# Optimization experiments

Measured on AMD Instinct MI355X. Metric: run time of the kernel, lower is better.

Reference implementation:

```python
import math
import jax, jax.numpy as jnp
import numpy as np

V, BS, L, C, H, B, T = 50257, 2048, 4, 768, 12, 2, 2048
D = C // H


def layer_norm(x, g, b, eps=1e-5):
    m = x.mean(-1, keepdims=True)
    v = ((x - m) ** 2).mean(-1, keepdims=True)
    return (x - m) / jnp.sqrt(v + eps) * g + b


def setup_inputs() -> dict:
    key = jax.random.key(0)
    ks = jax.random.split(key, 10)
    s = 0.02
    inp = {}
    inp["idx"] = jax.random.randint(ks[0], (B, T), 0, V)
    inp["tok_emb"] = jax.random.normal(ks[1], (V, C), jnp.float32) * s
    inp["pos_emb"] = jax.random.normal(ks[2], (BS, C), jnp.float32) * s
    inp["ln1_g"] = jnp.ones((L, C)); inp["ln1_b"] = jnp.zeros((L, C))
    inp["qkv_w"] = jax.random.normal(ks[3], (L, C, 3 * C), jnp.float32) * s
    inp["qkv_b"] = jnp.zeros((L, 3 * C))
    inp["aproj_w"] = jax.random.normal(ks[4], (L, C, C), jnp.float32) * s
    inp["aproj_b"] = jnp.zeros((L, C))
    inp["ln2_g"] = jnp.ones((L, C)); inp["ln2_b"] = jnp.zeros((L, C))
    inp["fc_w"] = jax.random.normal(ks[5], (L, C, 4 * C), jnp.float32) * s
    inp["fc_b"] = jnp.zeros((L, 4 * C))
    inp["mproj_w"] = jax.random.normal(ks[6], (L, 4 * C, C), jnp.float32) * s
    inp["mproj_b"] = jnp.zeros((L, C))
    inp["lnf_g"] = jnp.ones((C,)); inp["lnf_b"] = jnp.zeros((C,))
    inp["head_w"] = jax.random.normal(ks[7], (C, V), jnp.float32) * s
    return inp


def reference(idx, tok_emb, pos_emb, ln1_g, ln1_b, qkv_w, qkv_b, aproj_w, aproj_b,
              ln2_g, ln2_b, fc_w, fc_b, mproj_w, mproj_b, lnf_g, lnf_b, head_w):
    b, t = idx.shape
    x = tok_emb[idx] + pos_emb[:t][None]  # [B,T,C]; dropout p=0 -> identity
    mask = jnp.tril(jnp.ones((t, t), bool))  # causal
    neg_inf = jnp.finfo(x.dtype).min
    n_layer = qkv_w.shape[0]
    for l in range(n_layer):
        h = layer_norm(x, ln1_g[l], ln1_b[l])
        qkv = h @ qkv_w[l] + qkv_b[l]  # [B,T,3C]
        q, k, v = jnp.split(qkv, 3, axis=-1)
        q = q.reshape(b, t, H, D).transpose(0, 2, 1, 3)  # [B,H,T,D]
        k = k.reshape(b, t, H, D).transpose(0, 2, 1, 3)
        v = v.reshape(b, t, H, D).transpose(0, 2, 1, 3)
        att = jnp.einsum('bhqd,bhkd->bhqk', q, k) / math.sqrt(D)
        att = jnp.where(mask, att, neg_inf)
        att = jax.nn.softmax(att, axis=-1)
        y = jnp.einsum('bhqk,bhkd->bhqd', att, v)
        y = y.transpose(0, 2, 1, 3).reshape(b, t, C)
        x = x + (y @ aproj_w[l] + aproj_b[l])
        h2 = layer_norm(x, ln2_g[l], ln2_b[l])
        hid = jax.nn.gelu(h2 @ fc_w[l] + fc_b[l], approximate=False)  # exact erf GELU (torch default)
        x = x + (hid @ mproj_w[l] + mproj_b[l])
    x = layer_norm(x, lnf_g, lnf_b)
    logits = x @ head_w  # [B,T,V]
    return logits
```

## Files before the change

kernel.cpp:

```cpp
#include <hip/hip_runtime.h>
#include <cstdint>
#include <cstddef>

#define Tn 2048
#define Bn 2
#define Hn 12
#define Cn 768
#define Ln 4
#define Vn 50257

typedef unsigned short ushort_t;
typedef __attribute__((ext_vector_type(8))) __bf16 bf16x8;
typedef __attribute__((ext_vector_type(8))) unsigned short u16x8;
typedef __attribute__((ext_vector_type(4))) unsigned short u16x4;
typedef __attribute__((ext_vector_type(4))) float f32x4;

static constexpr size_t QKV_ELEMS = (size_t)Bn * Hn * Tn * 64;
static constexpr size_t OFF_QKV = 0;
static constexpr size_t OFF_APROJ = 1769472;
static constexpr size_t OFF_FC = 2359296;
static constexpr size_t OFF_MPROJ = 4718592;

__device__ inline unsigned short f2bf(float f) {
  unsigned int u = __float_as_uint(f);
  unsigned int r = (u + 0x7fffu + ((u >> 16) & 1u)) >> 16;
  return (unsigned short)r;
}

__device__ inline f32x4 zero4() { f32x4 z; z[0]=0.f; z[1]=0.f; z[2]=0.f; z[3]=0.f; return z; }

__device__ inline void gload_lds16(const ushort_t* g, ushort_t* l) {
  __builtin_amdgcn_global_load_lds(
      (const __attribute__((address_space(1))) void*)g,
      (__attribute__((address_space(3))) void*)l, 16, 0, 0);
}

__device__ inline int swz_lin() {
  int nbm = gridDim.x;
  int lin = blockIdx.y * nbm + blockIdx.x;
  int nwg = nbm * gridDim.y;
  int q = nwg >> 3, r = nwg & 7, x = lin & 7, p = lin >> 3;
  return (x < r ? x * (q + 1) : r * (q + 1) + (x - r) * q) + p;
}

__global__ __launch_bounds__(192) void embed_kernel(const int* __restrict__ idx,
    const float* __restrict__ tok, const float* __restrict__ pos, float* __restrict__ x) {
  int row = blockIdx.x;
  int t = row & (Tn - 1);
  int token = idx[row];
  const f32x4* tr = (const f32x4*)(tok + (size_t)token * Cn);
  const f32x4* pr = (const f32x4*)(pos + (size_t)t * Cn);
  f32x4* xr = (f32x4*)(x + (size_t)row * Cn);
  xr[threadIdx.x] = tr[threadIdx.x] + pr[threadIdx.x];
}

__global__ __launch_bounds__(256) void ln_kernel(const float* __restrict__ x,
    const float* __restrict__ gam, const float* __restrict__ bet, ushort_t* __restrict__ out) {
  const int wv = threadIdx.x >> 6, lane = threadIdx.x & 63;
  const int row = blockIdx.x * 4 + wv;
  const f32x4* xr = (const f32x4*)(x + (size_t)row * Cn);
  f32x4 v[3]; float s = 0.f, s2 = 0.f;
  #pragma unroll
  for (int e = 0; e < 3; ++e) {
    v[e] = xr[lane + e*64];
    #pragma unroll
    for (int j = 0; j < 4; ++j) { s += v[e][j]; s2 += v[e][j]*v[e][j]; }
  }
  #pragma unroll
  for (int off = 32; off >= 1; off >>= 1) { s += __shfl_xor(s, off); s2 += __shfl_xor(s2, off); }
  float mean = s * (1.f / Cn);
  float var  = s2 * (1.f / Cn) - mean * mean;
  float rstd = rsqrtf(var + 1e-5f);
  const f32x4* g4 = (const f32x4*)gam;
  const f32x4* b4 = (const f32x4*)bet;
  u16x4* o4 = (u16x4*)(out + (size_t)row * Cn);
  #pragma unroll
  for (int e = 0; e < 3; ++e) {
    f32x4 gv = g4[lane + e*64], bv = b4[lane + e*64];
    u16x4 o;
    #pragma unroll
    for (int j = 0; j < 4; ++j) o[j] = f2bf((v[e][j] - mean) * rstd * gv[j] + bv[j]);
    o4[lane + e*64] = o;
  }
}

__global__ __launch_bounds__(256) void tcvt_kernel(const float* __restrict__ in,
    ushort_t* __restrict__ out, int K, int N, int Npad) {
  __shared__ float tile[32][33];
  int n0 = blockIdx.x * 32, k0 = blockIdx.y * 32;
  int tx = threadIdx.x, ty = threadIdx.y;
  #pragma unroll
  for (int r = 0; r < 4; ++r) {
    int k = k0 + ty + 8*r;
    int n = n0 + tx;
    tile[ty + 8*r][tx] = (n < N) ? in[(size_t)k * N + n] : 0.f;
  }
  __syncthreads();
  #pragma unroll
  for (int r = 0; r < 4; ++r) {
    int n = n0 + ty + 8*r;
    out[(size_t)n * K + k0 + tx] = f2bf(tile[tx][ty + 8*r]);
  }
}

__global__ __launch_bounds__(256) void tcvt4_kernel(const float* __restrict__ qkvp,
    const float* __restrict__ aprojp, const float* __restrict__ fcp,
    const float* __restrict__ mprojp, ushort_t* __restrict__ wT) {
  __shared__ float tile[32][33];
  int bid = blockIdx.x;
  const float* in; int K, N, tilesX, local; size_t ooff;
  if (bid < 1728)      { in = qkvp;   K = 768;  N = 2304; tilesX = 72; ooff = OFF_QKV;   local = bid; }
  else if (bid < 2304) { in = aprojp; K = 768;  N = 768;  tilesX = 24; ooff = OFF_APROJ; local = bid - 1728; }
  else if (bid < 4608) { in = fcp;    K = 768;  N = 3072; tilesX = 96; ooff = OFF_FC;    local = bid - 2304; }
  else                 { in = mprojp; K = 3072; N = 768;  tilesX = 24; ooff = OFF_MPROJ; local = bid - 4608; }
  int n0 = (local % tilesX) * 32, k0 = (local / tilesX) * 32;
  int tx = threadIdx.x, ty = threadIdx.y;
  ushort_t* out = wT + ooff;
  #pragma unroll
  for (int r = 0; r < 4; ++r)
    tile[ty + 8*r][tx] = in[(size_t)(k0 + ty + 8*r) * N + n0 + tx];
  __syncthreads();
  #pragma unroll
  for (int r = 0; r < 4; ++r)
    out[(size_t)(n0 + ty + 8*r) * K + k0 + tx] = f2bf(tile[tx][ty + 8*r]);
}

__global__ __launch_bounds__(256) void vtrans_kernel(const ushort_t* __restrict__ vin,
                                                     ushort_t* __restrict__ vout) {
  __shared__ ushort_t tile[64][65];
  int t0 = blockIdx.x * 64;
  size_t bh = blockIdx.y;
  const ushort_t* src = vin + (bh * Tn + t0) * 64;
  int row = threadIdx.x >> 2, c0 = (threadIdx.x & 3) * 16;
  u16x8 a = *(const u16x8*)&src[(size_t)row * 64 + c0];
  u16x8 b = *(const u16x8*)&src[(size_t)row * 64 + c0 + 8];
  #pragma unroll
  for (int j = 0; j < 8; ++j) { tile[row][c0 + j] = a[j]; tile[row][c0 + 8 + j] = b[j]; }
  __syncthreads();
  int d = threadIdx.x >> 2, tq = (threadIdx.x & 3) * 16;
  u16x8 o0, o1;
  #pragma unroll
  for (int j = 0; j < 8; ++j) { o0[j] = tile[tq + j][d]; o1[j] = tile[tq + 8 + j][d]; }
  ushort_t* dst = vout + (bh * 64 + d) * Tn + t0 + tq;
  *(u16x8*)&dst[0] = o0;
  *(u16x8*)&dst[8] = o1;
}

__global__ __launch_bounds__(512, 2) void gemm256_kernel(
    const ushort_t* __restrict__ A, const ushort_t* __restrict__ Bt,
    const float* __restrict__ bias, float* __restrict__ outp,
    int M, int N, int K) {
  __shared__ ushort_t lds[3 * 16384];
  const int t = threadIdx.x;
  const int w = t >> 6, l = t & 63, lo = l & 15, g = l >> 4;
  const int wm = w >> 2, wn = w & 3;

  int bm, bn;
  {
    int seq = swz_lin();
    int gsz = 8 * gridDim.y;
    int grp = seq / gsz;
    int t2 = seq - grp * gsz;
    bn = t2 >> 3;
    bm = grp * 8 + (t2 & 7);
  }

  const ushort_t* gAb = A  + (size_t)bm * 256 * K;
  const ushort_t* gBb = Bt + (size_t)bn * 256 * K;

  f32x4 acc[8][4];
  #pragma unroll
  for (int i = 0; i < 8; ++i)
    #pragma unroll
    for (int j = 0; j < 4; ++j) acc[i][j] = zero4();

  auto stage = [&](int kt, int buf) {
    const int k0 = kt << 5;
    #pragma unroll
    for (int j = 0; j < 2; ++j) {
      const int q = j * 512 + t;
      const int r = q >> 2;
      const int cc = ((q & 3) ^ ((r >> 1) & 3)) << 3;
      gload_lds16(gAb + (size_t)r * K + k0 + cc,
                  &lds[buf * 16384 + j * 4096 + w * 512]);
      gload_lds16(gBb + (size_t)r * K + k0 + cc,
                  &lds[buf * 16384 + 8192 + j * 4096 + w * 512]);
    }
  };
  const int csw = ((lo >> 1) & 3) << 3;
  auto compute = [&](int buf) {
    const ushort_t* as = &lds[buf * 16384];
    const ushort_t* bs = &lds[buf * 16384 + 8192];
    bf16x8 af[8], bfr[4];
    #pragma unroll
    for (int mi = 0; mi < 8; ++mi)
      af[mi] = *(const bf16x8*)&as[(wm*128 + mi*16 + lo) * 32 + ((g*8) ^ csw)];
    #pragma unroll
    for (int ni = 0; ni < 4; ++ni)
      bfr[ni] = *(const bf16x8*)&bs[(wn*64 + ni*16 + lo) * 32 + ((g*8) ^ csw)];
    __builtin_amdgcn_s_setprio(1);
    #pragma unroll
    for (int mi = 0; mi < 8; ++mi)
      #pragma unroll
      for (int ni = 0; ni < 4; ++ni)
        acc[mi][ni] = __builtin_amdgcn_mfma_f32_16x16x32_bf16(af[mi], bfr[ni], acc[mi][ni], 0, 0, 0);
    __builtin_amdgcn_s_setprio(0);
  };

  const int NK = K >> 5;
  stage(0, 0); stage(1, 1); stage(2, 2);
  asm volatile("s_waitcnt vmcnt(8)" ::: "memory");
  __builtin_amdgcn_s_barrier();

  int buf = 0;
  #pragma unroll 1
  for (int kt = 0; kt < NK; ++kt) {
    compute(buf);
    asm volatile("s_waitcnt lgkmcnt(0)" ::: "memory");
    __builtin_amdgcn_s_barrier();
    if (kt + 3 < NK) {
      stage(kt + 3, buf);
      asm volatile("s_waitcnt vmcnt(8)" ::: "memory");
    } else if (kt + 2 < NK) {
      asm volatile("s_waitcnt vmcnt(4)" ::: "memory");
    } else {
      asm volatile("s_waitcnt vmcnt(0)" ::: "memory");
    }
    __builtin_amdgcn_s_barrier();
    buf = (buf == 2) ? 0 : buf + 1;
  }

  #pragma unroll
  for (int mi = 0; mi < 8; ++mi) {
    #pragma unroll
    for (int ni = 0; ni < 4; ++ni) {
      int colg = bn*256 + wn*64 + ni*16 + lo;
      if (colg < N) {
        float bv = bias ? bias[colg] : 0.f;
        #pragma unroll
        for (int i = 0; i < 4; ++i) {
          int rowg = bm*256 + wm*128 + mi*16 + 4*g + i;
          outp[(size_t)rowg * N + colg] = acc[mi][ni][i] + bv;
        }
      }
    }
  }
}

template<int MODE, int TM>
__global__ __launch_bounds__(256) void gemm_kernel(
    const ushort_t* __restrict__ A, const ushort_t* __restrict__ Bt,
    const float* __restrict__ bias, void* __restrict__ outp,
    const float* __restrict__ res, int M, int N, int K) {
  constexpr int MI = TM / 32;
  constexpr int ASZ = TM * 32;
  constexpr int BUFE = ASZ + 4096;
  constexpr int LPT = TM/64 + 2;
  __shared__ ushort_t lds[3 * BUFE];
  const int t = threadIdx.x;
  int bm, bn;
  {
    int seq = swz_lin();
    const int G = 8;
    int gsz = G * gridDim.y;
    int grp = seq / gsz;
    int t2 = seq - grp * gsz;
    bn = t2 / G;
    bm = grp * G + (t2 - bn * G);
  }
  const int w = t >> 6, l = t & 63, lo = l & 15, g = l >> 4;
  const int wm = w >> 1, wn = w & 1;

  f32x4 acc[MI][4];
  #pragma unroll
  for (int i = 0; i < MI; ++i)
    #pragma unroll
    for (int j = 0; j < 4; ++j) acc[i][j] = zero4();

  const ushort_t* gAb = A  + (size_t)bm * TM * K;
  const ushort_t* gBb = Bt + (size_t)bn * 128 * K;

  auto stage = [&](int kt, int buf) {
    const int k0 = kt << 5;
    #pragma unroll
    for (int j = 0; j < TM/64; ++j) {
      const int q = j * 256 + t;
      const int r = q >> 2;
      const int cc = ((q & 3) ^ ((r >> 1) & 3)) << 3;
      gload_lds16(gAb + (size_t)r * K + k0 + cc, &lds[buf*BUFE + (j*256 + w*64)*8]);
    }
    #pragma unroll
    for (int j = 0; j < 2; ++j) {
      const int q = j * 256 + t;
      const int r = q >> 2;
      const int cc = ((q & 3) ^ ((r >> 1) & 3)) << 3;
      gload_lds16(gBb + (size_t)r * K + k0 + cc, &lds[buf*BUFE + ASZ + (j*256 + w*64)*8]);
    }
  };
  const int csw = ((lo >> 1) & 3) << 3;
  auto compute = [&](int buf) {
    const ushort_t* as = &lds[buf * BUFE];
    const ushort_t* bs = &lds[buf * BUFE + ASZ];
    bf16x8 af[MI], bfr[4];
    #pragma unroll
    for (int mi = 0; mi < MI; ++mi)
      af[mi] = *(const bf16x8*)&as[(wm*(TM/2) + mi*16 + lo) * 32 + ((g*8) ^ csw)];
    #pragma unroll
    for (int ni = 0; ni < 4; ++ni)
      bfr[ni] = *(const bf16x8*)&bs[(wn*64 + ni*16 + lo) * 32 + ((g*8) ^ csw)];
    __builtin_amdgcn_s_setprio(1);
    #pragma unroll
    for (int mi = 0; mi < MI; ++mi)
      #pragma unroll
      for (int ni = 0; ni < 4; ++ni)
        acc[mi][ni] = __builtin_amdgcn_mfma_f32_16x16x32_bf16(af[mi], bfr[ni], acc[mi][ni], 0, 0, 0);
    __builtin_amdgcn_s_setprio(0);
  };

  const int NK = K >> 5;
  stage(0, 0); stage(1, 1); stage(2, 2);
  if constexpr (LPT == 4) asm volatile("s_waitcnt vmcnt(8)" ::: "memory");
  else                    asm volatile("s_waitcnt vmcnt(6)" ::: "memory");
  __builtin_amdgcn_s_barrier();

  int buf = 0;
  #pragma unroll 1
  for (int kt = 0; kt < NK; ++kt) {
    compute(buf);
    asm volatile("s_waitcnt lgkmcnt(0)" ::: "memory");
    __builtin_amdgcn_s_barrier();
    if (kt + 3 < NK) {
      stage(kt + 3, buf);
      if constexpr (LPT == 4) asm volatile("s_waitcnt vmcnt(8)" ::: "memory");
      else                    asm volatile("s_waitcnt vmcnt(6)" ::: "memory");
    } else if (kt + 2 < NK) {
      if constexpr (LPT == 4) asm volatile("s_waitcnt vmcnt(4)" ::: "memory");
      else                    asm volatile("s_waitcnt vmcnt(3)" ::: "memory");
    } else {
      asm volatile("s_waitcnt vmcnt(0)" ::: "memory");
    }
    __builtin_amdgcn_s_barrier();
    buf = (buf == 2) ? 0 : buf + 1;
  }

  #pragma unroll
  for (int mi = 0; mi < MI; ++mi) {
    #pragma unroll
    for (int ni = 0; ni < 4; ++ni) {
      int colg = bn*128 + wn*64 + ni*16 + lo;
      if (colg < N) {
        float bv = bias ? bias[colg] : 0.f;
        #pragma unroll
        for (int i = 0; i < 4; ++i) {
          int rowg = bm*TM + wm*(TM/2) + mi*16 + 4*g + i;
          float vv = acc[mi][ni][i] + bv;
          if (MODE == 1) {
            size_t off = (size_t)rowg * N + colg;
            ((float*)outp)[off] = res[off] + vv;
          } else if (MODE == 2) {
            float ge = 0.5f * vv * (1.f + erff(vv * 0.70710678118f));
            ((ushort_t*)outp)[(size_t)rowg * N + colg] = f2bf(ge);
          } else {
            int which = colg / Cn;
            int rem = colg - which * Cn;
            int h = rem >> 6, d = rem & 63;
            int b = rowg >> 11, tt = rowg & (Tn - 1);
            ushort_t* qb = (ushort_t*)outp;
            size_t bh = (size_t)(b * Hn + h);
            size_t off = (bh * Tn + tt) * 64 + d;
            if (which == 0)      qb[off] = f2bf(vv * 0.125f);
            else if (which == 1) qb[QKV_ELEMS + off] = f2bf(vv);
            else                 qb[3*QKV_ELEMS + off] = f2bf(vv);
          }
        }
      }
    }
  }
}

__global__ __launch_bounds__(64) void attn_kernel(const ushort_t* __restrict__ qkvh,
                                                  ushort_t* __restrict__ y) {
  const int l = threadIdx.x;
  const int lo = l & 15, g = l >> 4;
  int nl = swz_lin();
  const int qt = nl & 127;
  const int bh = nl >> 7;
  const int b = bh / Hn, h = bh % Hn;
  const int q0 = qt * 16;
  const ushort_t* Qp = qkvh + (size_t)bh * Tn * 64;
  const ushort_t* Kp = qkvh + QKV_ELEMS + (size_t)bh * Tn * 64;
  const ushort_t* Vt = qkvh + 2*QKV_ELEMS + (size_t)bh * 64 * Tn;

  bf16x8 qf[2];
  #pragma unroll
  for (int ch = 0; ch < 2; ++ch)
    qf[ch] = *(const bf16x8*)&Qp[(size_t)(q0 + lo) * 64 + ch*32 + g*8];

  f32x4 of[4];
  #pragma unroll
  for (int ch = 0; ch < 4; ++ch) of[ch] = zero4();
  float m = -1e30f, lsum = 0.f;
  const int nkv = q0 + 16;
  const bool ghi = (g >= 2);
  const int lg2 = (g & 1) * 32;

  for (int kv0 = 0; kv0 < nkv; kv0 += 32) {
    bf16x8 vf[4];
    #pragma unroll
    for (int ch = 0; ch < 4; ++ch)
      vf[ch] = *(const bf16x8*)&Vt[(size_t)(ch*16 + lo) * Tn + kv0 + g*8];

    float s8[8];
    #pragma unroll
    for (int sub = 0; sub < 2; ++sub) {
      int kvb = kv0 + 16*sub;
      bf16x8 kf[2];
      #pragma unroll
      for (int ch = 0; ch < 2; ++ch)
        kf[ch] = *(const bf16x8*)&Kp[(size_t)(kvb + lo) * 64 + ch*32 + g*8];
      f32x4 st = zero4();
      st = __builtin_amdgcn_mfma_f32_16x16x32_bf16(kf[0], qf[0], st, 0, 0, 0);
      st = __builtin_amdgcn_mfma_f32_16x16x32_bf16(kf[1], qf[1], st, 0, 0, 0);
      #pragma unroll
      for (int i = 0; i < 4; ++i) {
        int kvi = kvb + 4*g + i;
        s8[sub*4 + i] = (kvi <= q0 + lo) ? st[i] : -1e30f;
      }
    }
    float tmax = s8[0];
    #pragma unroll
    for (int j = 1; j < 8; ++j) tmax = fmaxf(tmax, s8[j]);
    tmax = fmaxf(tmax, __shfl_xor(tmax, 16));
    tmax = fmaxf(tmax, __shfl_xor(tmax, 32));
    if (!__all(tmax <= m)) {
      float newm = fmaxf(m, tmax);
      float resc = __expf(m - newm);
      lsum *= resc;
      m = newm;
      #pragma unroll
      for (int i = 0; i < 4; ++i) {
        float rs = __shfl(resc, 4*g + i);
        of[0][i] *= rs; of[1][i] *= rs; of[2][i] *= rs; of[3][i] *= rs;
      }
    }
    float p8[8]; float psum = 0.f;
    #pragma unroll
    for (int j = 0; j < 8; ++j) { p8[j] = __expf(s8[j] - m); psum += p8[j]; }
    psum += __shfl_xor(psum, 16);
    psum += __shfl_xor(psum, 32);
    lsum += psum;
    unsigned int q4[4];
    #pragma unroll
    for (int c = 0; c < 4; ++c)
      asm("v_cvt_pk_bf16_f32 %0, %1, %2" : "=v"(q4[c]) : "v"(p8[2*c]), "v"(p8[2*c+1]));
    union { unsigned int wv[4]; bf16x8 v; } pu;
    #pragma unroll
    for (int j = 0; j < 4; ++j) {
      int srcLane = lo + lg2 + ((j >> 1) << 4);
      unsigned int lo_w = (unsigned int)__shfl((int)q4[j & 1], srcLane);
      unsigned int hi_w = (unsigned int)__shfl((int)q4[2 + (j & 1)], srcLane);
      pu.wv[j] = ghi ? hi_w : lo_w;
    }
    #pragma unroll
    for (int ch = 0; ch < 4; ++ch)
      of[ch] = __builtin_amdgcn_mfma_f32_16x16x32_bf16(pu.v, vf[ch], of[ch], 0, 0, 0);
  }

  #pragma unroll
  for (int i = 0; i < 4; ++i) {
    float li = 1.f / __shfl(lsum, 4*g + i);
    of[0][i] *= li; of[1][i] *= li; of[2][i] *= li; of[3][i] *= li;
  }
  ushort_t* yb = y + ((size_t)b*Tn + q0) * Cn + h*64;
  #pragma unroll
  for (int ch = 0; ch < 4; ++ch)
    #pragma unroll
    for (int i = 0; i < 4; ++i)
      yb[(size_t)(4*g + i) * Cn + ch*16 + lo] = f2bf(of[ch][i]);
}

extern "C" void kernel_launch(void* const* d_in, const int* in_sizes, int n_in,
                              void* d_out, int out_size, void* d_ws, size_t ws_size,
                              hipStream_t stream) {
  const int*   idx     = (const int*)d_in[0];
  const float* tok_emb = (const float*)d_in[1];
  const float* pos_emb = (const float*)d_in[2];
  const float* ln1_g   = (const float*)d_in[3];
  const float* ln1_b   = (const float*)d_in[4];
  const float* qkv_w   = (const float*)d_in[5];
  const float* qkv_b   = (const float*)d_in[6];
  const float* aproj_w = (const float*)d_in[7];
  const float* aproj_b = (const float*)d_in[8];
  const float* ln2_g   = (const float*)d_in[9];
  const float* ln2_b   = (const float*)d_in[10];
  const float* fc_w    = (const float*)d_in[11];
  const float* fc_b    = (const float*)d_in[12];
  const float* mproj_w = (const float*)d_in[13];
  const float* mproj_b = (const float*)d_in[14];
  const float* lnf_g   = (const float*)d_in[15];
  const float* lnf_b   = (const float*)d_in[16];
  const float* head_w  = (const float*)d_in[17];
  float* out = (float*)d_out;

  char* ws = (char*)d_ws;
  float*    x    = (float*)(ws);
  ushort_t* hA   = (ushort_t*)(ws + 12582912);
  ushort_t* hB   = (ushort_t*)(ws + 18874368);
  ushort_t* qkvh = (ushort_t*)(ws + 44040192);
  ushort_t* wT   = (ushort_t*)(ws + 69206016);

  const int M = Bn * Tn;
  dim3 tb(32, 8);

  embed_kernel<<<M, 192, 0, stream>>>(idx, tok_emb, pos_emb, x);
  for (int l = 0; l < Ln; ++l) {
    ln_kernel<<<M/4, 256, 0, stream>>>(x, ln1_g + l*Cn, ln1_b + l*Cn, hA);
    tcvt4_kernel<<<6912, tb, 0, stream>>>(qkv_w + (size_t)l*Cn*3*Cn, aproj_w + (size_t)l*Cn*Cn,
                                          fc_w + (size_t)l*Cn*4*Cn, mproj_w + (size_t)l*4*Cn*Cn, wT);
    gemm_kernel<3,128><<<dim3(M/128, 2304/128), 256, 0, stream>>>(hA, wT + OFF_QKV, qkv_b + (size_t)l*3*Cn, qkvh, nullptr, M, 2304, 768);
    vtrans_kernel<<<dim3(Tn/64, Bn*Hn), 256, 0, stream>>>(qkvh + 3*QKV_ELEMS, qkvh + 2*QKV_ELEMS);
    attn_kernel<<<dim3(128, Bn*Hn), 64, 0, stream>>>(qkvh, hA);
    gemm_kernel<1,64><<<dim3(M/64, 768/128), 256, 0, stream>>>(hA, wT + OFF_APROJ, aproj_b + (size_t)l*Cn, x, x, M, 768, 768);
    ln_kernel<<<M/4, 256, 0, stream>>>(x, ln2_g + l*Cn, ln2_b + l*Cn, hA);
    gemm_kernel<2,128><<<dim3(M/128, 3072/128), 256, 0, stream>>>(hA, wT + OFF_FC, fc_b + (size_t)l*4*Cn, hB, nullptr, M, 3072, 768);
    gemm_kernel<1,64><<<dim3(M/64, 768/128), 256, 0, stream>>>(hB, wT + OFF_MPROJ, mproj_b + (size_t)l*Cn, x, x, M, 768, 3072);
  }
  ln_kernel<<<M/4, 256, 0, stream>>>(x, lnf_g, lnf_b, hA);
  tcvt_kernel<<<dim3(50432/32, 768/32), tb, 0, stream>>>(head_w, wT, 768, Vn, 50432);
  gemm256_kernel<<<dim3(M/256, 50432/256), 512, 0, stream>>>(hA, wT, nullptr, out, M, Vn, 768);
}
```

Baseline: 1.691 ms.

## Batch weight conversion for all layers, reorder attention tiles, use generic GEMM for head

Weights for all four layers are transposed and converted to bf16 in one launch before the loop, replacing one launch per layer. Attention blocks are reversed so the longest causal query tiles get scheduled first, which should balance load across compute units. The specialised 256x256 LM-head GEMM is removed and the head projection goes through the generic 128-tile gemm_kernel with a new plain-store mode. That head GEMM dominates the runtime, so dropping the tuned kernel risks lower throughput there.

New measurement: 1.694 ms. No clear change (+0.2%).

```diff
diff --git a/kernel.cpp b/kernel.cpp
--- a/kernel.cpp
+++ b/kernel.cpp
@@ -20,6 +20,7 @@
 static constexpr size_t OFF_APROJ = 1769472;
 static constexpr size_t OFF_FC = 2359296;
 static constexpr size_t OFF_MPROJ = 4718592;
+static constexpr size_t PACK_SZ = 7077888;
 
 __device__ inline unsigned short f2bf(float f) {
   unsigned int u = __float_as_uint(f);
@@ -103,19 +104,21 @@
   }
 }
 
-__global__ __launch_bounds__(256) void tcvt4_kernel(const float* __restrict__ qkvp,
-    const float* __restrict__ aprojp, const float* __restrict__ fcp,
-    const float* __restrict__ mprojp, ushort_t* __restrict__ wT) {
+__global__ __launch_bounds__(256) void tcvtAll_kernel(const float* __restrict__ qkvw,
+    const float* __restrict__ aprojw, const float* __restrict__ fcw,
+    const float* __restrict__ mprojw, ushort_t* __restrict__ wT) {
   __shared__ float tile[32][33];
   int bid = blockIdx.x;
-  const float* in; int K, N, tilesX, local; size_t ooff;
-  if (bid < 1728)      { in = qkvp;   K = 768;  N = 2304; tilesX = 72; ooff = OFF_QKV;   local = bid; }
-  else if (bid < 2304) { in = aprojp; K = 768;  N = 768;  tilesX = 24; ooff = OFF_APROJ; local = bid - 1728; }
-  else if (bid < 4608) { in = fcp;    K = 768;  N = 3072; tilesX = 96; ooff = OFF_FC;    local = bid - 2304; }
-  else                 { in = mprojp; K = 3072; N = 768;  tilesX = 24; ooff = OFF_MPROJ; local = bid - 4608; }
+  const int layer = bid / 6912;
+  int local = bid - layer * 6912;
+  const float* in; int K, N, tilesX; size_t ooff;
+  if (local < 1728)      { in = qkvw   + (size_t)layer*1769472; K = 768;  N = 2304; tilesX = 72; ooff = OFF_QKV; }
+  else if (local < 2304) { in = aprojw + (size_t)layer*589824;  K = 768;  N = 768;  tilesX = 24; ooff = OFF_APROJ; local -= 1728; }
+  else if (local < 4608) { in = fcw    + (size_t)layer*2359296; K = 768;  N = 3072; tilesX = 96; ooff = OFF_FC;    local -= 2304; }
+  else                   { in = mprojw + (size_t)layer*2359296; K = 3072; N = 768;  tilesX = 24; ooff = OFF_MPROJ; local -= 4608; }
   int n0 = (local % tilesX) * 32, k0 = (local / tilesX) * 32;
   int tx = threadIdx.x, ty = threadIdx.y;
-  ushort_t* out = wT + ooff;
+  ushort_t* out = wT + (size_t)layer * PACK_SZ + ooff;
   #pragma unroll
   for (int r = 0; r < 4; ++r)
     tile[ty + 8*r][tx] = in[(size_t)(k0 + ty + 8*r) * N + n0 + tx];
@@ -144,107 +147,6 @@
   ushort_t* dst = vout + (bh * 64 + d) * Tn + t0 + tq;
   *(u16x8*)&dst[0] = o0;
   *(u16x8*)&dst[8] = o1;
-}
-
-__global__ __launch_bounds__(512, 2) void gemm256_kernel(
-    const ushort_t* __restrict__ A, const ushort_t* __restrict__ Bt,
-    const float* __restrict__ bias, float* __restrict__ outp,
-    int M, int N, int K) {
-  __shared__ ushort_t lds[3 * 16384];
-  const int t = threadIdx.x;
-  const int w = t >> 6, l = t & 63, lo = l & 15, g = l >> 4;
-  const int wm = w >> 2, wn = w & 3;
-
-  int bm, bn;
-  {
-    int seq = swz_lin();
-    int gsz = 8 * gridDim.y;
-    int grp = seq / gsz;
-    int t2 = seq - grp * gsz;
-    bn = t2 >> 3;
-    bm = grp * 8 + (t2 & 7);
-  }
-
-  const ushort_t* gAb = A  + (size_t)bm * 256 * K;
-  const ushort_t* gBb = Bt + (size_t)bn * 256 * K;
-
-  f32x4 acc[8][4];
-  #pragma unroll
-  for (int i = 0; i < 8; ++i)
-    #pragma unroll
-    for (int j = 0; j < 4; ++j) acc[i][j] = zero4();
-
-  auto stage = [&](int kt, int buf) {
-    const int k0 = kt << 5;
-    #pragma unroll
-    for (int j = 0; j < 2; ++j) {
-      const int q = j * 512 + t;
-      const int r = q >> 2;
-      const int cc = ((q & 3) ^ ((r >> 1) & 3)) << 3;
-      gload_lds16(gAb + (size_t)r * K + k0 + cc,
-                  &lds[buf * 16384 + j * 4096 + w * 512]);
-      gload_lds16(gBb + (size_t)r * K + k0 + cc,
-                  &lds[buf * 16384 + 8192 + j * 4096 + w * 512]);
-    }
-  };
-  const int csw = ((lo >> 1) & 3) << 3;
-  auto compute = [&](int buf) {
-    const ushort_t* as = &lds[buf * 16384];
-    const ushort_t* bs = &lds[buf * 16384 + 8192];
-    bf16x8 af[8], bfr[4];
-    #pragma unroll
-    for (int mi = 0; mi < 8; ++mi)
-      af[mi] = *(const bf16x8*)&as[(wm*128 + mi*16 + lo) * 32 + ((g*8) ^ csw)];
-    #pragma unroll
-    for (int ni = 0; ni < 4; ++ni)
-      bfr[ni] = *(const bf16x8*)&bs[(wn*64 + ni*16 + lo) * 32 + ((g*8) ^ csw)];
-    __builtin_amdgcn_s_setprio(1);
-    #pragma unroll
-    for (int mi = 0; mi < 8; ++mi)
-      #pragma unroll
-      for (int ni = 0; ni < 4; ++ni)
-        acc[mi][ni] = __builtin_amdgcn_mfma_f32_16x16x32_bf16(af[mi], bfr[ni], acc[mi][ni], 0, 0, 0);
-    __builtin_amdgcn_s_setprio(0);
-  };
-
-  const int NK = K >> 5;
-  stage(0, 0); stage(1, 1); stage(2, 2);
-  asm volatile("s_waitcnt vmcnt(8)" ::: "memory");
-  __builtin_amdgcn_s_barrier();
-
-  int buf = 0;
-  #pragma unroll 1
-  for (int kt = 0; kt < NK; ++kt) {
-    compute(buf);
-    asm volatile("s_waitcnt lgkmcnt(0)" ::: "memory");
-    __builtin_amdgcn_s_barrier();
-    if (kt + 3 < NK) {
-      stage(kt + 3, buf);
-      asm volatile("s_waitcnt vmcnt(8)" ::: "memory");
-    } else if (kt + 2 < NK) {
-      asm volatile("s_waitcnt vmcnt(4)" ::: "memory");
-    } else {
-      asm volatile("s_waitcnt vmcnt(0)" ::: "memory");
-    }
-    __builtin_amdgcn_s_barrier();
-    buf = (buf == 2) ? 0 : buf + 1;
-  }
-
-  #pragma unroll
-  for (int mi = 0; mi < 8; ++mi) {
-    #pragma unroll
-    for (int ni = 0; ni < 4; ++ni) {
-      int colg = bn*256 + wn*64 + ni*16 + lo;
-      if (colg < N) {
-        float bv = bias ? bias[colg] : 0.f;
-        #pragma unroll
-        for (int i = 0; i < 4; ++i) {
-          int rowg = bm*256 + wm*128 + mi*16 + 4*g + i;
-          outp[(size_t)rowg * N + colg] = acc[mi][ni][i] + bv;
-        }
-      }
-    }
-  }
 }
 
 template<int MODE, int TM>
@@ -354,7 +256,9 @@
         for (int i = 0; i < 4; ++i) {
           int rowg = bm*TM + wm*(TM/2) + mi*16 + 4*g + i;
           float vv = acc[mi][ni][i] + bv;
-          if (MODE == 1) {
+          if (MODE == 0) {
+            ((float*)outp)[(size_t)rowg * N + colg] = vv;
+          } else if (MODE == 1) {
             size_t off = (size_t)rowg * N + colg;
             ((float*)outp)[off] = res[off] + vv;
           } else if (MODE == 2) {
@@ -383,7 +287,7 @@
   const int l = threadIdx.x;
   const int lo = l & 15, g = l >> 4;
   int nl = swz_lin();
-  const int qt = nl & 127;
+  const int qt = 127 - (nl & 127);
   const int bh = nl >> 7;
   const int b = bh / Hn, h = bh % Hn;
   const int q0 = qt * 16;
@@ -513,19 +417,19 @@
   dim3 tb(32, 8);
 
   embed_kernel<<<M, 192, 0, stream>>>(idx, tok_emb, pos_emb, x);
+  tcvtAll_kernel<<<27648, tb, 0, stream>>>(qkv_w, aproj_w, fc_w, mproj_w, wT);
   for (int l = 0; l < Ln; ++l) {
+    ushort_t* wTl = wT + (size_t)l * PACK_SZ;
     ln_kernel<<<M/4, 256, 0, stream>>>(x, ln1_g + l*Cn, ln1_b + l*Cn, hA);
-    tcvt4_kernel<<<6912, tb, 0, stream>>>(qkv_w + (size_t)l*Cn*3*Cn, aproj_w + (size_t)l*Cn*Cn,
-                                          fc_w + (size_t)l*Cn*4*Cn, mproj_w + (size_t)l*4*Cn*Cn, wT);
-    gemm_kernel<3,128><<<dim3(M/128, 2304/128), 256, 0, stream>>>(hA, wT + OFF_QKV, qkv_b + (size_t)l*3*Cn, qkvh, nullptr, M, 2304, 768);
+    gemm_kernel<3,128><<<dim3(M/128, 2304/128), 256, 0, stream>>>(hA, wTl + OFF_QKV, qkv_b + (size_t)l*3*Cn, qkvh, nullptr, M, 2304, 768);
     vtrans_kernel<<<dim3(Tn/64, Bn*Hn), 256, 0, stream>>>(qkvh + 3*QKV_ELEMS, qkvh + 2*QKV_ELEMS);
     attn_kernel<<<dim3(128, Bn*Hn), 64, 0, stream>>>(qkvh, hA);
-    gemm_kernel<1,64><<<dim3(M/64, 768/128), 256, 0, stream>>>(hA, wT + OFF_APROJ, aproj_b + (size_t)l*Cn, x, x, M, 768, 768);
+    gemm_kernel<1,64><<<dim3(M/64, 768/128), 256, 0, stream>>>(hA, wTl + OFF_APROJ, aproj_b + (size_t)l*Cn, x, x, M, 768, 768);
     ln_kernel<<<M/4, 256, 0, stream>>>(x, ln2_g + l*Cn, ln2_b + l*Cn, hA);
-    gemm_kernel<2,128><<<dim3(M/128, 3072/128), 256, 0, stream>>>(hA, wT + OFF_FC, fc_b + (size_t)l*4*Cn, hB, nullptr, M, 3072, 768);
-    gemm_kernel<1,64><<<dim3(M/64, 768/128), 256, 0, stream>>>(hB, wT + OFF_MPROJ, mproj_b + (size_t)l*Cn, x, x, M, 768, 3072);
+    gemm_kernel<2,128><<<dim3(M/128, 3072/128), 256, 0, stream>>>(hA, wTl + OFF_FC, fc_b + (size_t)l*4*Cn, hB, nullptr, M, 3072, 768);
+    gemm_kernel<1,64><<<dim3(M/64, 768/128), 256, 0, stream>>>(hB, wTl + OFF_MPROJ, mproj_b + (size_t)l*Cn, x, x, M, 768, 3072);
   }
   ln_kernel<<<M/4, 256, 0, stream>>>(x, lnf_g, lnf_b, hA);
   tcvt_kernel<<<dim3(50432/32, 768/32), tb, 0, stream>>>(head_w, wT, 768, Vn, 50432);
-  gemm256_kernel<<<dim3(M/256, 50432/256), 512, 0, stream>>>(hA, wT, nullptr, out, M, Vn, 768);
-}
+  gemm_kernel<0,128><<<dim3(M/128, 50432/128), 256, 0, stream>>>(hA, wT, nullptr, out, nullptr, M, Vn, 768);
+}
```
